# Optimization experiments

Hardware: AMD Instinct MI355X
Metric: run time of the kernel (lower is better)

The kernel has to match this reference:

```python
import jax, jax.numpy as jnp
import numpy as np

DIM = 64
HEADS = 8
GLOBAL_HEADS = 4   # heads - local_attn_heads
DIM_HEAD = 64
INNER = HEADS * DIM_HEAD  # 512
NB_FEATURES = int(DIM_HEAD * np.log(DIM_HEAD))  # 266, performer_pytorch default
NUM_TOKENS = 64
VOCAB = 26
B, N = 8, 2048


def _orth_gauss(m, d, rng):
    # gaussian orthogonal random matrix (scaling=0), as in performer_pytorch
    blocks = []
    for _ in range(int(np.ceil(m / d))):
        q, _ = np.linalg.qr(rng.normal(size=(d, d)))
        blocks.append(q.T)
    mat = np.concatenate(blocks, 0)[:m]
    mult = np.linalg.norm(rng.normal(size=(m, d)), axis=1)
    return (mult[:, None] * mat).astype(np.float32)


def _layernorm(x, g, b, eps=1e-5):
    mu = x.mean(-1, keepdims=True)
    var = jnp.mean((x - mu) ** 2, axis=-1, keepdims=True)
    return (x - mu) / jnp.sqrt(var + eps) * g + b


def _fixed_pos_emb(n, dim):
    inv_freq = 1.0 / (10000.0 ** (jnp.arange(0, dim, 2, dtype=jnp.float32) / dim))
    t = jnp.arange(n, dtype=jnp.float32)[:, None] * inv_freq[None, :]
    return jnp.concatenate([jnp.sin(t), jnp.cos(t)], axis=-1)  # [n, dim]


def _rotate_every_two(x):
    x1, x2 = x[..., ::2], x[..., 1::2]
    return jnp.stack((-x2, x1), axis=-1).reshape(x.shape)


def _apply_rotary(q, k, sinu):
    half = sinu.shape[-1] // 2
    sin = jnp.repeat(sinu[:, :half], 2, axis=-1)
    cos = jnp.repeat(sinu[:, half:], 2, axis=-1)
    rot = lambda t: t * cos + _rotate_every_two(t) * sin
    return rot(q), rot(k)


def _softmax_kernel(x, proj, is_query, eps=1e-4):
    # FAVOR+ positive softmax random features
    dn = x.shape[-1] ** -0.25
    ratio = proj.shape[0] ** -0.5
    dash = jnp.einsum('bhnd,md->bhnm', x * dn, proj)
    diag = jnp.sum(x * x, axis=-1, keepdims=True) * (0.5 * dn * dn)
    mx = jnp.max(dash, axis=-1, keepdims=True) if is_query else jnp.max(dash)
    return ratio * (jnp.exp(dash - diag - mx) + eps)


def _forward(input_ids, tok_emb, ln1_g, ln1_b, Wq, Wk, Wv, Wo, ln2_g, ln2_b,
             W1, b1, W2, b2, lnf_g, lnf_b, Wout, bout, Wc1, bc1, Wc2, bc2, proj):
    b, n = input_ids.shape
    mask = input_ids != 0  # padding mask (pad id == 0)
    x = tok_emb[input_ids] + _fixed_pos_emb(n, DIM)[None]  # token + abs sinusoidal pos
    sinu = _fixed_pos_emb(n, DIM_HEAD)  # rotary table for attention heads

    def attn(h):
        hn = _layernorm(h, ln1_g, ln1_b)
        to_h = lambda W: (hn @ W).reshape(b, n, HEADS, DIM_HEAD).transpose(0, 2, 1, 3)
        q, k, v = to_h(Wq), to_h(Wk), to_h(Wv)  # [b,h,n,d]
        qg, ql = q[:, :GLOBAL_HEADS], q[:, GLOBAL_HEADS:]
        kg, kl = k[:, :GLOBAL_HEADS], k[:, GLOBAL_HEADS:]
        vg, vl = v[:, :GLOBAL_HEADS], v[:, GLOBAL_HEADS:]
        # --- global heads: FAVOR+ linear attention (rotary applied to global q/k only) ---
        vg = vg * mask[:, None, :, None]  # performer zeroes v at padded positions
        qg, kg = _apply_rotary(qg, kg, sinu)
        qp = _softmax_kernel(qg, proj, True)   # [b,h,n,m]
        kp = _softmax_kernel(kg, proj, False)
        ctx = jnp.einsum('bhnm,bhnd->bhmd', kp, vg)
        denom = jnp.einsum('bhnm,bhm->bhn', qp, kp.sum(axis=2))
        og = jnp.einsum('bhnm,bhmd->bhnd', qp, ctx) / denom[..., None]
        # --- local heads: window_size == seq_len -> exact softmax attn + key pad mask ---
        dots = jnp.einsum('bhnd,bhmd->bhnm', ql, kl) * (DIM_HEAD ** -0.5)
        dots = jnp.where(mask[:, None, None, :], dots, jnp.asarray(-1e9, dots.dtype))
        ol = jnp.einsum('bhnm,bhmd->bhnd', jax.nn.softmax(dots, axis=-1), vl)
        out = jnp.concatenate([og, ol], axis=1).transpose(0, 2, 1, 3).reshape(b, n, INNER)
        return out @ Wo

    def ff(h):
        hn = _layernorm(h, ln2_g, ln2_b)
        return jax.nn.gelu(hn @ W1 + b1, approximate=False) @ W2 + b2

    # reversible sequence, depth 1: x1 = x2 = x; output = mean of the two streams
    y1 = x + attn(x)
    y2 = x + ff(y1)
    h = _layernorm(0.5 * (y1 + y2), lnf_g, lnf_b)
    logits = h @ Wout + bout  # [b, n, NUM_TOKENS]
    rep = logits[:, 0, :]     # CLS slot, [b, 64]
    out = jax.nn.relu(rep @ Wc1 + bc1) @ Wc2 + bc2  # [b, 2]
    return out, rep


def setup_inputs():
    key = jax.random.key(0)
    ks = jax.random.split(key, 12)
    rng = np.random.default_rng(0)
    s = lambda k, shape, scale=0.05: jax.random.normal(k, shape, jnp.float32) * scale
    return {
        'input_ids': jax.random.randint(ks[0], (B, N), 0, VOCAB, dtype=jnp.int32),
        'tok_emb': s(ks[1], (NUM_TOKENS, DIM), 1.0),
        'ln1_g': jnp.ones((DIM,), jnp.float32), 'ln1_b': jnp.zeros((DIM,), jnp.float32),
        'Wq': s(ks[2], (DIM, INNER)), 'Wk': s(ks[3], (DIM, INNER)), 'Wv': s(ks[4], (DIM, INNER)),
        'Wo': s(ks[5], (INNER, DIM)),
        'ln2_g': jnp.ones((DIM,), jnp.float32), 'ln2_b': jnp.zeros((DIM,), jnp.float32),
        'W1': s(ks[6], (DIM, 4 * DIM)), 'b1': jnp.zeros((4 * DIM,), jnp.float32),
        'W2': s(ks[7], (4 * DIM, DIM)), 'b2': jnp.zeros((DIM,), jnp.float32),
        'lnf_g': jnp.ones((DIM,), jnp.float32), 'lnf_b': jnp.zeros((DIM,), jnp.float32),
        'Wout': s(ks[8], (DIM, NUM_TOKENS)), 'bout': jnp.zeros((NUM_TOKENS,), jnp.float32),
        'Wc1': s(ks[9], (DIM, 32)), 'bc1': jnp.zeros((32,), jnp.float32),
        'Wc2': s(ks[10], (32, 2)), 'bc2': jnp.zeros((2,), jnp.float32),
        'proj': jnp.asarray(_orth_gauss(NB_FEATURES, DIM_HEAD, rng)),
    }


def reference(input_ids, tok_emb, ln1_g, ln1_b, Wq, Wk, Wv, Wo, ln2_g, ln2_b,
              W1, b1, W2, b2, lnf_g, lnf_b, Wout, bout, Wc1, bc1, Wc2, bc2, proj):
    return _forward(input_ids, tok_emb, ln1_g, ln1_b, Wq, Wk, Wv, Wo, ln2_g, ln2_b,
                    W1, b1, W2, b2, lnf_g, lnf_b, Wout, bout, Wc1, bc1, Wc2, bc2, proj)
```

## Files before the change

### kernel.cpp

```cpp
#include <hip/hip_runtime.h>
#include <math.h>

#define NTOK 2048
#define NBF 266
#define MPAD 272
#define ZWORDS4 138843u

typedef unsigned short u16;
typedef __attribute__((ext_vector_type(8))) short short8;
typedef __attribute__((ext_vector_type(4))) float f32x4;

__device__ __forceinline__ float bf2f(u16 u) {
  unsigned int x = ((unsigned int)u) << 16;
  return __uint_as_float(x);
}
__device__ __forceinline__ u16 f2bf(float f) {
  unsigned int x = __float_as_uint(f);
  unsigned int r = x + 0x7FFFu + ((x >> 16) & 1u);
  return (u16)(r >> 16);
}
__device__ __forceinline__ float wredsum64(float v) {
  for (int o = 32; o > 0; o >>= 1) v += __shfl_xor(v, o);
  return v;
}
__device__ __forceinline__ float bsum256(float v, float* red) {
  for (int o = 32; o > 0; o >>= 1) v += __shfl_xor(v, o);
  __syncthreads();
  if ((threadIdx.x & 63) == 0) red[threadIdx.x >> 6] = v;
  __syncthreads();
  return red[0] + red[1] + red[2] + red[3];
}
__device__ __forceinline__ float bmax256(float v, float* red) {
  for (int o = 32; o > 0; o >>= 1) v = fmaxf(v, __shfl_xor(v, o));
  __syncthreads();
  if ((threadIdx.x & 63) == 0) red[threadIdx.x >> 6] = v;
  __syncthreads();
  return fmaxf(fmaxf(red[0], red[1]), fmaxf(red[2], red[3]));
}
#define INVF_C 0.4152410118609190f

__global__ __launch_bounds__(128) void k_prep(
    const int* __restrict__ ids, const float* __restrict__ tok_emb,
    const float* __restrict__ ln1g, const float* __restrict__ ln1b,
    const float* __restrict__ Wk, const float* __restrict__ Wv,
    u16* __restrict__ Kg, u16* __restrict__ Vg, u16* __restrict__ hng,
    float* __restrict__ diagK, float* __restrict__ x0,
    uint4* __restrict__ zbase) {
  int blk = blockIdx.x;
  int b = blk >> 8, nt = blk & 255;
  int n0 = nt * 8;
  int t = threadIdx.x;
  int w = t >> 6, lane = t & 63;
  __shared__ float hn[8][64];
  __shared__ float idm[8];
  __shared__ float2 sctab[256];

  {
    unsigned int zi = (unsigned int)blk * 128u + (unsigned int)t;
    if (zi < ZWORDS4) zbase[zi] = make_uint4(0u, 0u, 0u, 0u);
  }
#pragma unroll
  for (int p = 0; p < 2; ++p) {
    int ee = t + p * 128;
    int n = n0 + (ee >> 5), i = ee & 31;
    float ang = (float)n * exp2f(-INVF_C * (float)i);
    sctab[ee] = make_float2(sinf(ang), cosf(ang));
  }
  __syncthreads();

  float g = ln1g[lane], bb = ln1b[lane];
#pragma unroll
  for (int j2 = 0; j2 < 4; ++j2) {
    int j = w * 4 + j2;
    int n = n0 + j;
    int id = ids[b * NTOK + n];
    float2 p = sctab[(j << 5) + (lane & 31)];
    float pv = (lane < 32) ? p.x : p.y;
    float xv = tok_emb[id * 64 + lane] + pv;
    float mu = wredsum64(xv) * 0.015625f;
    float dv = xv - mu;
    float var = wredsum64(dv * dv) * 0.015625f;
    float hv = dv * rsqrtf(var + 1e-5f) * g + bb;
    hn[j][lane] = hv;
    hng[((size_t)b * NTOK + n) * 64 + lane] = f2bf(hv);
    if (lane == 0) idm[j] = (id != 0) ? 1.f : 0.f;
    if (n == 0) x0[b * 64 + lane] = xv;
  }
  __syncthreads();

  float acc[8][4];
#pragma unroll
  for (int j = 0; j < 8; ++j)
#pragma unroll
    for (int i = 0; i < 4; ++i) acc[j][i] = 0.f;
  const float* wsrc = (t < 64) ? (Wk + t * 4) : (Wv + (t - 64) * 4);
  for (int d2 = 0; d2 < 64; ++d2) {
    float4 w0 = *reinterpret_cast<const float4*>(wsrc + d2 * 512);
#pragma unroll
    for (int j = 0; j < 8; ++j) {
      float hv = hn[j][d2];
      acc[j][0] += hv * w0.x; acc[j][1] += hv * w0.y;
      acc[j][2] += hv * w0.z; acc[j][3] += hv * w0.w;
    }
  }

  if (t < 64) {
    int hh = t >> 4, db = (t & 15) * 4;
    int i0 = (t & 15) * 2;
#pragma unroll
    for (int j = 0; j < 8; ++j) {
      int n = n0 + j;
      float2 t0 = sctab[(j << 5) + i0];
      float2 t1 = sctab[(j << 5) + i0 + 1];
      float s0 = t0.x, c0 = t0.y, s1 = t1.x, c1 = t1.y;
      float kr0 = acc[j][0] * c0 - acc[j][1] * s0;
      float kr1 = acc[j][1] * c0 + acc[j][0] * s0;
      float kr2 = acc[j][2] * c1 - acc[j][3] * s1;
      float kr3 = acc[j][3] * c1 + acc[j][2] * s1;
      float dq = kr0 * kr0 + kr1 * kr1 + kr2 * kr2 + kr3 * kr3;
      dq += __shfl_xor(dq, 1);
      dq += __shfl_xor(dq, 2);
      dq += __shfl_xor(dq, 4);
      dq += __shfl_xor(dq, 8);
      size_t hb = (size_t)(b * 4 + hh) * NTOK + n;
      if ((t & 15) == 0) diagK[hb] = dq * 0.0625f;
      ushort4 s;
      s.x = f2bf(kr0); s.y = f2bf(kr1); s.z = f2bf(kr2); s.w = f2bf(kr3);
      *reinterpret_cast<ushort4*>(Kg + hb * 64 + db) = s;
    }
  } else {
    int tv = t - 64;
    int hh = tv >> 4, db = (tv & 15) * 4;
#pragma unroll
    for (int j = 0; j < 8; ++j) {
      int n = n0 + j;
      float m = idm[j];
      ushort4 vv;
      vv.x = f2bf(acc[j][0] * m); vv.y = f2bf(acc[j][1] * m);
      vv.z = f2bf(acc[j][2] * m); vv.w = f2bf(acc[j][3] * m);
      *reinterpret_cast<ushort4*>(
          Vg + ((size_t)(b * 4 + hh) * NTOK + n) * 64 + db) = vv;
    }
  }
}

__device__ __forceinline__ void stage_prj(const float* __restrict__ proj,
                                          u16* prjbf, int t, int m0, int rows) {
  for (int c = t; c < rows * 8; c += 256) {
    int r = c >> 3, k0 = (c & 7) * 8;
    int m = m0 + r;
    int e = (r * 64 + k0) ^ ((r & 7) << 3);
    uint4 pk;
    if (m < NBF) {
      const float4* ps = reinterpret_cast<const float4*>(proj + m * 64 + k0);
      float4 p0 = ps[0], p1 = ps[1];
      pk.x = (unsigned)f2bf(p0.x) | ((unsigned)f2bf(p0.y) << 16);
      pk.y = (unsigned)f2bf(p0.z) | ((unsigned)f2bf(p0.w) << 16);
      pk.z = (unsigned)f2bf(p1.x) | ((unsigned)f2bf(p1.y) << 16);
      pk.w = (unsigned)f2bf(p1.z) | ((unsigned)f2bf(p1.w) << 16);
    } else {
      pk.x = pk.y = pk.z = pk.w = 0u;
    }
    *reinterpret_cast<uint4*>(&prjbf[e]) = pk;
  }
}

__global__ __launch_bounds__(256) void k_max(
    const u16* __restrict__ Kg, const float* __restrict__ proj,
    unsigned int* __restrict__ gmax) {
  int bh = blockIdx.x, ns = blockIdx.y;
  int t = threadIdx.x, lane = t & 63, w = t >> 6;
  __shared__ __align__(16) u16 prjbf[MPAD * 64];
  __shared__ __align__(16) u16 kbf[64 * 64];
  __shared__ float red[4];
  stage_prj(proj, prjbf, t, 0, MPAD);
  float mv = -3e38f;
  int ko = (lane >> 4) * 8;
  for (int c4 = 0; c4 < 2; ++c4) {
    int nb = ns * 128 + c4 * 64;
    __syncthreads();
    for (int p = 0; p < 2; ++p) {
      int idx = t + p * 256;
      int n = idx >> 3, k0 = (idx & 7) * 8;
      uint4 src = *reinterpret_cast<const uint4*>(
          Kg + ((size_t)bh * NTOK + nb + n) * 64 + k0);
      *reinterpret_cast<uint4*>(&kbf[(n * 64 + k0) ^ ((n & 7) << 3)]) = src;
    }
    __syncthreads();
    int nl = w * 16 + (lane & 15);
    short8 a0 = *reinterpret_cast<const short8*>(&kbf[(nl * 64 + ko) ^ ((nl & 7) << 3)]);
    short8 a1 = *reinterpret_cast<const short8*>(&kbf[(nl * 64 + ko + 32) ^ ((nl & 7) << 3)]);
#pragma unroll
    for (int mt = 0; mt < 17; ++mt) {
      int m = mt * 16 + (lane & 15);
      short8 b0 = *reinterpret_cast<const short8*>(&prjbf[(m * 64 + ko) ^ ((m & 7) << 3)]);
      short8 b1 = *reinterpret_cast<const short8*>(&prjbf[(m * 64 + ko + 32) ^ ((m & 7) << 3)]);
      f32x4 d = {0.f, 0.f, 0.f, 0.f};
      d = __builtin_amdgcn_mfma_f32_16x16x32_bf16(a0, b0, d, 0, 0, 0);
      d = __builtin_amdgcn_mfma_f32_16x16x32_bf16(a1, b1, d, 0, 0, 0);
      if (m < NBF) {
        mv = fmaxf(mv, fmaxf(fmaxf(d[0], d[1]), fmaxf(d[2], d[3])));
      }
    }
  }
  mv *= 0.35355339059327373f;
  for (int o = 32; o > 0; o >>= 1) mv = fmaxf(mv, __shfl_xor(mv, o));
  __syncthreads();
  if (lane == 0) red[w] = mv;
  __syncthreads();
  if (t == 0) {
    float m2 = fmaxf(fmaxf(red[0], red[1]), fmaxf(red[2], red[3]));
    unsigned int b = __float_as_uint(m2);
    unsigned int u = (b & 0x80000000u) ? ~b : (b | 0x80000000u);
    atomicMax(gmax, u);
  }
}

__global__ __launch_bounds__(256) void k_ctx(
    const u16* __restrict__ Kg, const u16* __restrict__ Vg,
    const float* __restrict__ diagK, const float* __restrict__ proj,
    const unsigned int* __restrict__ gmax,
    float* __restrict__ ctx, float* __restrict__ ksum) {
  int bh = blockIdx.x, ns = blockIdx.y, mz = blockIdx.z;
  int m0 = mz * 144;
  int nmt = mz ? 8 : 9;
  int t = threadIdx.x, lane = t & 63, w = t >> 6;
  __shared__ __align__(16) u16 prjbf[144 * 64];
  __shared__ __align__(16) u16 kpT[144 * 64];
  __shared__ __align__(16) u16 kbf[64 * 64];
  __shared__ __align__(16) u16 vbT[64 * 64];
  __shared__ float dg[64];
  __shared__ float ksl[144];
  stage_prj(proj, prjbf, t, m0, 144);
  if (t < 144) ksl[t] = 0.f;
  unsigned int u = *gmax;
  unsigned int bb = (u & 0x80000000u) ? (u & 0x7FFFFFFFu) : ~u;
  float mx = __uint_as_float(bb);
  const float dn = 0.35355339059327373f;
  const float ratio = 1.0f / sqrtf(266.0f);
  int ko = (lane >> 4) * 8;
  f32x4 acc[9];
  float ksacc[9];
#pragma unroll
  for (int i = 0; i < 9; ++i) { acc[i] = (f32x4){0.f, 0.f, 0.f, 0.f}; ksacc[i] = 0.f; }

  for (int c4 = 0; c4 < 4; ++c4) {
    int nb = ns * 256 + c4 * 64;
    for (int p = 0; p < 2; ++p) {
      int idx = t + p * 256;
      int n = idx >> 3, k0 = (idx & 7) * 8;
      uint4 src = *reinterpret_cast<const uint4*>(
          Kg + ((size_t)bh * NTOK + nb + n) * 64 + k0);
      *reinterpret_cast<uint4*>(&kbf[(n * 64 + k0) ^ ((n & 7) << 3)]) = src;
      uint4 vv = *reinterpret_cast<const uint4*>(
          Vg + ((size_t)bh * NTOK + nb + n) * 64 + k0);
      u16 pv[8];
      *reinterpret_cast<uint4*>(pv) = vv;
#pragma unroll
      for (int i = 0; i < 8; ++i) {
        int d = k0 + i;
        vbT[(d * 64 + n) ^ ((d & 7) << 3)] = pv[i];
      }
    }
    if (t < 64) dg[t] = diagK[(size_t)bh * NTOK + nb + t];
    __syncthreads();
    {
      int nl = w * 16 + (lane & 15);
      short8 a0 = *reinterpret_cast<const short8*>(&kbf[(nl * 64 + ko) ^ ((nl & 7) << 3)]);
      short8 a1 = *reinterpret_cast<const short8*>(&kbf[(nl * 64 + ko + 32) ^ ((nl & 7) << 3)]);
      float dgv[4];
#pragma unroll
      for (int r = 0; r < 4; ++r) dgv[r] = dg[w * 16 + (lane >> 4) * 4 + r];
      int n0 = w * 16 + (lane >> 4) * 4;
#pragma unroll
      for (int mt = 0; mt < 9; ++mt) {
        if (mt < nmt) {
          int lr = mt * 16 + (lane & 15);
          short8 b0 = *reinterpret_cast<const short8*>(&prjbf[(lr * 64 + ko) ^ ((lr & 7) << 3)]);
          short8 b1 = *reinterpret_cast<const short8*>(&prjbf[(lr * 64 + ko + 32) ^ ((lr & 7) << 3)]);
          f32x4 d = {0.f, 0.f, 0.f, 0.f};
          d = __builtin_amdgcn_mfma_f32_16x16x32_bf16(a0, b0, d, 0, 0, 0);
          d = __builtin_amdgcn_mfma_f32_16x16x32_bf16(a1, b1, d, 0, 0, 0);
          float kp0 = ratio * (expf(dn * d[0] - dgv[0] - mx) + 1e-4f);
          float kp1 = ratio * (expf(dn * d[1] - dgv[1] - mx) + 1e-4f);
          float kp2 = ratio * (expf(dn * d[2] - dgv[2] - mx) + 1e-4f);
          float kp3 = ratio * (expf(dn * d[3] - dgv[3] - mx) + 1e-4f);
          ushort4 pkk;
          pkk.x = f2bf(kp0); pkk.y = f2bf(kp1); pkk.z = f2bf(kp2); pkk.w = f2bf(kp3);
          *reinterpret_cast<ushort4*>(&kpT[(lr * 64 + n0) ^ ((lr & 7) << 3)]) = pkk;
          float ksp = kp0 + kp1 + kp2 + kp3;
          ksp += __shfl_xor(ksp, 16);
          ksp += __shfl_xor(ksp, 32);
          ksacc[mt] += ksp;
        }
      }
    }
    __syncthreads();
    {
      int dcol = w * 16 + (lane & 15);
      short8 vb0 = *reinterpret_cast<const short8*>(&vbT[(dcol * 64 + ko) ^ ((dcol & 7) << 3)]);
      short8 vb1 = *reinterpret_cast<const short8*>(&vbT[(dcol * 64 + ko + 32) ^ ((dcol & 7) << 3)]);
#pragma unroll
      for (int mt = 0; mt < 9; ++mt) {
        if (mt < nmt) {
          int lr = mt * 16 + (lane & 15);
          short8 a0 = *reinterpret_cast<const short8*>(&kpT[(lr * 64 + ko) ^ ((lr & 7) << 3)]);
          short8 a1 = *reinterpret_cast<const short8*>(&kpT[(lr * 64 + ko + 32) ^ ((lr & 7) << 3)]);
          acc[mt] = __builtin_amdgcn_mfma_f32_16x16x32_bf16(a0, vb0, acc[mt], 0, 0, 0);
          acc[mt] = __builtin_amdgcn_mfma_f32_16x16x32_bf16(a1, vb1, acc[mt], 0, 0, 0);
        }
      }
    }
    __syncthreads();
  }
  int dcol = w * 16 + (lane & 15);
#pragma unroll
  for (int mt = 0; mt < 9; ++mt) {
    if (mt < nmt) {
#pragma unroll
      for (int r = 0; r < 4; ++r) {
        int m = m0 + mt * 16 + (lane >> 4) * 4 + r;
        if (m < NBF)
          atomicAdd(&ctx[((size_t)bh * NBF + m) * 64 + dcol], acc[mt][r]);
      }
      if (lane < 16) atomicAdd(&ksl[mt * 16 + lane], ksacc[mt]);
    }
  }
  __syncthreads();
  if (t < 144 && m0 + t < NBF)
    atomicAdd(&ksum[(size_t)bh * NBF + m0 + t], ksl[t]);
}

__global__ __launch_bounds__(256) void k_att(
    const int* __restrict__ ids,
    const float* __restrict__ ln1g, const float* __restrict__ ln1b,
    const float* __restrict__ Wq, const float* __restrict__ Wk,
    const float* __restrict__ Wv, const float* __restrict__ proj,
    const u16* __restrict__ hng,
    const float* __restrict__ ctx, const float* __restrict__ ksum,
    const float* __restrict__ x0,
    const float* __restrict__ ln2g, const float* __restrict__ ln2b,
    const float* __restrict__ Wo,
    const float* __restrict__ W1, const float* __restrict__ b1,
    const float* __restrict__ W2, const float* __restrict__ b2,
    const float* __restrict__ lnfg, const float* __restrict__ lnfb,
    const float* __restrict__ Wout, const float* __restrict__ bout,
    const float* __restrict__ Wc1, const float* __restrict__ bc1,
    const float* __restrict__ Wc2, const float* __restrict__ bc2,
    float* __restrict__ att, float* __restrict__ svecG,
    float* __restrict__ sdenG, unsigned int* __restrict__ cnt,
    float* __restrict__ out) {
  int b = blockIdx.x, y = blockIdx.y;
  int t = threadIdx.x, lane = t & 63, wg = t >> 6;
  __shared__ float hn1[64], qh[64], qpart[4][64], red[4], pol[4][64];
  __shared__ float buf[272];
  __shared__ __align__(16) u16 vst[512 * 64];
  __shared__ float pbuf[512];
  __shared__ float wkq[64];
  __shared__ int lastf;
  __shared__ float fo512[512], fx0[64], fy1[64], fhn2[64], fgact[256];
  __shared__ float fhfin[64], frep[64], fc1[32], fsd[4];
  const float dn = 0.35355339059327373f;
  const float ratio = 1.0f / sqrtf(266.0f);
  int h = (y < 4) ? y : (4 + ((y - 4) >> 2));

  if (t < 64) {
    float xv = x0[b * 64 + t];
    float mu = wredsum64(xv) * 0.015625f;
    float dv = xv - mu;
    float var = wredsum64(dv * dv) * 0.015625f;
    hn1[t] = dv * rsqrtf(var + 1e-5f) * ln1g[t] + ln1b[t];
  }
  __syncthreads();
  {
    float p = 0;
#pragma unroll
    for (int dd = 0; dd < 16; ++dd)
      p += hn1[wg * 16 + dd] * Wq[(wg * 16 + dd) * 512 + h * 64 + lane];
    qpart[wg][lane] = p;
  }
  __syncthreads();
  if (t < 64) qh[t] = qpart[0][t] + qpart[1][t] + qpart[2][t] + qpart[3][t];
  __syncthreads();

  if (y < 4) {
    int bh = b * 4 + h;
    float dq = 0;
#pragma unroll
    for (int d = 0; d < 64; ++d) dq += qh[d] * qh[d];
    dq *= 0.0625f;
    float lmax = -3e38f;
#pragma unroll
    for (int pass = 0; pass < 2; ++pass) {
      int m = t + pass * 256;
      if (m < NBF) {
        const float4* pp = reinterpret_cast<const float4*>(proj + m * 64);
        float s = 0;
#pragma unroll
        for (int q4 = 0; q4 < 16; ++q4) {
          float4 uu = pp[q4];
          s += qh[q4 * 4] * uu.x + qh[q4 * 4 + 1] * uu.y +
               qh[q4 * 4 + 2] * uu.z + qh[q4 * 4 + 3] * uu.w;
        }
        float dash = dn * s;
        buf[m] = dash;
        lmax = fmaxf(lmax, dash);
      }
    }
    float mxq = bmax256(lmax, red);
    float part = 0;
#pragma unroll
    for (int pass = 0; pass < 2; ++pass) {
      int m = t + pass * 256;
      if (m < NBF) {
        float qp = ratio * (expf(buf[m] - dq - mxq) + 1e-4f);
        buf[m] = qp;
        part += qp * ksum[(size_t)bh * NBF + m];
      }
    }
    float den = bsum256(part, red);
    __syncthreads();
    {
      float s = 0;
      for (int m = wg; m < NBF; m += 4)
        s += buf[m] * ctx[((size_t)bh * NBF + m) * 64 + lane];
      pol[wg][lane] = s;
    }
    __syncthreads();
    if (t < 64)
      att[b * 512 + h * 64 + t] =
          (pol[0][t] + pol[1][t] + pol[2][t] + pol[3][t]) / den;
  } else {
    int hl = (y - 4) >> 2, sl = (y - 4) & 3;
    int ch = (4 + hl) * 64;
    {
      float p = 0;
#pragma unroll
      for (int jj = 0; jj < 16; ++jj)
        p += Wk[lane * 512 + ch + wg * 16 + jj] * qh[wg * 16 + jj];
      qpart[wg][lane] = p;
    }
    __syncthreads();
    if (t < 64) wkq[t] = qpart[0][t] + qpart[1][t] + qpart[2][t] + qpart[3][t];
    const u16* hnb = hng + ((size_t)b * NTOK + sl * 512) * 64;
    for (int p = 0; p < 16; ++p) {
      int idx = t + p * 256;
      int r = idx >> 3, k0 = (idx & 7) * 8;
      uint4 src = *reinterpret_cast<const uint4*>(hnb + (size_t)r * 64 + k0);
      *reinterpret_cast<uint4*>(&vst[(r * 64 + k0) ^ ((r & 7) << 3)]) = src;
    }
    __syncthreads();
    float ps = 0;
#pragma unroll
    for (int i = 0; i < 2; ++i) {
      int r = t + i * 256;
      float s = 0;
#pragma unroll
      for (int c8 = 0; c8 < 8; ++c8) {
        uint4 uu = *reinterpret_cast<const uint4*>(
            &vst[(r * 64 + c8 * 8) ^ ((r & 7) << 3)]);
        u16 pv[8];
        *reinterpret_cast<uint4*>(pv) = uu;
#pragma unroll
        for (int k = 0; k < 8; ++k) s += wkq[c8 * 8 + k] * bf2f(pv[k]);
      }
      float p = (ids[b * NTOK + sl * 512 + r] == 0) ? 0.f : expf(s * 0.125f);
      pbuf[r] = p;
      ps += p;
    }
    float psb = bsum256(ps, red);
    if (t == 0) atomicAdd(&sdenG[b * 4 + hl], psb);
    float acc = 0;
    int r0 = wg * 128;
#pragma unroll 8
    for (int r = 0; r < 128; ++r)
      acc += pbuf[r0 + r] * bf2f(vst[((r0 + r) * 64 + lane) ^ (((r0 + r) & 7) << 3)]);
    pol[wg][lane] = acc;
    __syncthreads();
    if (t < 64)
      atomicAdd(&svecG[(b * 4 + hl) * 64 + t],
                pol[0][t] + pol[1][t] + pol[2][t] + pol[3][t]);
  }

  __syncthreads();
  if (t == 0) {
    __threadfence();
    unsigned int prev = atomicAdd(&cnt[b], 1u);
    lastf = (prev == 19u) ? 1 : 0;
  }
  __syncthreads();
  if (!lastf) return;
  __threadfence();

  if (t < 4) fsd[t] = sdenG[b * 4 + t];
  {
    int hh = t >> 6, j = t & 63;
    float s = 0;
#pragma unroll 8
    for (int d = 0; d < 64; ++d)
      s += svecG[(b * 4 + hh) * 64 + d] * Wv[d * 512 + 256 + hh * 64 + j];
    pol[hh][j] = s;
  }
  if (t < 256) fo512[t] = att[b * 512 + t];
  if (t < 64) fx0[t] = x0[b * 64 + t];
  __syncthreads();
  {
    int hh = t >> 6, j = t & 63;
    fo512[256 + hh * 64 + j] = pol[hh][j] / fsd[hh];
  }
  __syncthreads();
  {
    float s = 0;
#pragma unroll 4
    for (int c = wg * 128; c < wg * 128 + 128; ++c) s += fo512[c] * Wo[c * 64 + lane];
    pol[wg][lane] = s;
  }
  __syncthreads();
  if (t < 64) {
    float yv = fx0[t] + pol[0][t] + pol[1][t] + pol[2][t] + pol[3][t];
    fy1[t] = yv;
    float mu = wredsum64(yv) * 0.015625f;
    float dv = yv - mu;
    float var = wredsum64(dv * dv) * 0.015625f;
    fhn2[t] = dv * rsqrtf(var + 1e-5f) * ln2g[t] + ln2b[t];
  }
  __syncthreads();
  {
    float s = b1[t];
#pragma unroll 4
    for (int d = 0; d < 64; ++d) s += fhn2[d] * W1[d * 256 + t];
    fgact[t] = 0.5f * s * (1.f + erff(s * 0.7071067811865475f));
  }
  __syncthreads();
  {
    float s = 0;
#pragma unroll 4
    for (int j = wg * 64; j < wg * 64 + 64; ++j) s += fgact[j] * W2[j * 64 + lane];
    pol[wg][lane] = s;
  }
  __syncthreads();
  if (t < 64) {
    float y2 = fx0[t] + b2[t] + pol[0][t] + pol[1][t] + pol[2][t] + pol[3][t];
    float hm = 0.5f * (fy1[t] + y2);
    float mu = wredsum64(hm) * 0.015625f;
    float dv = hm - mu;
    float var = wredsum64(dv * dv) * 0.015625f;
    fhfin[t] = dv * rsqrtf(var + 1e-5f) * lnfg[t] + lnfb[t];
  }
  __syncthreads();
  {
    float s = 0;
#pragma unroll
    for (int dd = 0; dd < 16; ++dd)
      s += fhfin[wg * 16 + dd] * Wout[(wg * 16 + dd) * 64 + lane];
    pol[wg][lane] = s;
  }
  __syncthreads();
  if (t < 64) {
    float s = bout[t] + pol[0][t] + pol[1][t] + pol[2][t] + pol[3][t];
    frep[t] = s;
    out[16 + b * 64 + t] = s;
  }
  __syncthreads();
  if (t < 32) {
    float s = bc1[t];
#pragma unroll 4
    for (int d = 0; d < 64; ++d) s += frep[d] * Wc1[d * 32 + t];
    fc1[t] = fmaxf(s, 0.f);
  }
  __syncthreads();
  if (t < 2) {
    float s = bc2[t];
#pragma unroll
    for (int jj = 0; jj < 32; ++jj) s += fc1[jj] * Wc2[jj * 2 + t];
    out[b * 2 + t] = s;
  }
}

extern "C" void kernel_launch(void* const* d_in, const int* in_sizes, int n_in,
                              void* d_out, int out_size, void* d_ws, size_t ws_size,
                              hipStream_t stream) {
  (void)in_sizes; (void)n_in; (void)out_size; (void)ws_size;
  const int* ids = (const int*)d_in[0];
  const float* tok = (const float*)d_in[1];
  const float* ln1g = (const float*)d_in[2];
  const float* ln1b = (const float*)d_in[3];
  const float* Wq = (const float*)d_in[4];
  const float* Wk = (const float*)d_in[5];
  const float* Wv = (const float*)d_in[6];
  const float* Wo = (const float*)d_in[7];
  const float* ln2g = (const float*)d_in[8];
  const float* ln2b = (const float*)d_in[9];
  const float* W1 = (const float*)d_in[10];
  const float* b1 = (const float*)d_in[11];
  const float* W2 = (const float*)d_in[12];
  const float* b2 = (const float*)d_in[13];
  const float* lnfg = (const float*)d_in[14];
  const float* lnfb = (const float*)d_in[15];
  const float* Wout = (const float*)d_in[16];
  const float* bout = (const float*)d_in[17];
  const float* Wc1 = (const float*)d_in[18];
  const float* bc1 = (const float*)d_in[19];
  const float* Wc2 = (const float*)d_in[20];
  const float* bc2 = (const float*)d_in[21];
  const float* proj = (const float*)d_in[22];

  uint8_t* w = (uint8_t*)d_ws;
  size_t off = 0;
  const size_t big = (size_t)8 * 4 * NTOK * 64 * 2;
  u16* Kg = (u16*)(w + off); off += big;
  u16* Vg = (u16*)(w + off); off += big;
  u16* hng = (u16*)(w + off); off += (size_t)8 * NTOK * 64 * 2;
  float* diagK = (float*)(w + off); off += (size_t)8 * 4 * NTOK * 4;
  float* ctx = (float*)(w + off); off += (size_t)8 * 4 * NBF * 64 * 4;
  float* ksum = (float*)(w + off); off += (size_t)8 * 4 * NBF * 4;
  float* svecG = (float*)(w + off); off += (size_t)8 * 4 * 64 * 4;
  float* sdenG = (float*)(w + off); off += (size_t)8 * 4 * 4;
  unsigned int* gmax = (unsigned int*)(w + off); off += 4;
  unsigned int* cnt = (unsigned int*)(w + off); off += 32;
  off += 12;
  float* x0 = (float*)(w + off); off += 64 * 8 * 4;
  float* att = (float*)(w + off); off += (size_t)8 * 512 * 4;

  k_prep<<<8 * 256, 128, 0, stream>>>(ids, tok, ln1g, ln1b, Wk, Wv, Kg, Vg, hng,
                                      diagK, x0, (uint4*)ctx);
  k_max<<<dim3(32, 16), 256, 0, stream>>>(Kg, proj, gmax);
  k_ctx<<<dim3(32, 8, 2), 256, 0, stream>>>(Kg, Vg, diagK, proj, gmax, ctx, ksum);
  k_att<<<dim3(8, 20), 256, 0, stream>>>(ids, ln1g, ln1b, Wq, Wk, Wv, proj, hng,
                                         ctx, ksum, x0, ln2g, ln2b, Wo, W1, b1,
                                         W2, b2, lnfg, lnfb, Wout, bout, Wc1,
                                         bc1, Wc2, bc2, att, svecG, sdenG, cnt,
                                         (float*)d_out);
}
```

Baseline: 114.8 us.

## Move local-attention blocks into the context kernel to overlap with FAVOR work

The local-head attention blocks, which compute the query projection, scores over a 512-token slice and the weighted value sum, move out of the final attention kernel into extra z-slices of the context kernel. They now run alongside the FAVOR+ context accumulation, and the final kernel launches only 4 global-head blocks per batch, with the last-block counter adjusted to match. The context kernel's shared memory is merged into a single 64KB buffer reused by both paths. This shortens the serialized tail kernel, at the cost of a larger context-kernel grid with many early-exit blocks and higher shared memory per block, which may lower occupancy.

```diff
diff --git a/kernel.cpp b/kernel.cpp
--- a/kernel.cpp
+++ b/kernel.cpp
@@ -220,17 +220,100 @@
     const u16* __restrict__ Kg, const u16* __restrict__ Vg,
     const float* __restrict__ diagK, const float* __restrict__ proj,
     const unsigned int* __restrict__ gmax,
-    float* __restrict__ ctx, float* __restrict__ ksum) {
+    float* __restrict__ ctx, float* __restrict__ ksum,
+    const int* __restrict__ ids,
+    const float* __restrict__ ln1g, const float* __restrict__ ln1b,
+    const float* __restrict__ Wq, const float* __restrict__ Wk,
+    const float* __restrict__ x0, const u16* __restrict__ hng,
+    float* __restrict__ svecG, float* __restrict__ sdenG) {
   int bh = blockIdx.x, ns = blockIdx.y, mz = blockIdx.z;
+  int t = threadIdx.x, lane = t & 63, w = t >> 6;
+  __shared__ __align__(16) unsigned char bigbuf[65536];
+  __shared__ float dg[64];
+  __shared__ float ksl[144];
+  __shared__ float hn1[64], qh[64], wkq[64], qpart[4][64], red[4], pol[4][64];
+  __shared__ float pbuf[512];
+
+  if (mz == 2) {
+    if (ns >= 4) return;
+    int b = bh >> 2, hl = bh & 3, sl = ns;
+    int ch = (4 + hl) * 64;
+    u16* vst = (u16*)bigbuf;
+    if (t < 64) {
+      float xv = x0[b * 64 + t];
+      float mu = wredsum64(xv) * 0.015625f;
+      float dv = xv - mu;
+      float var = wredsum64(dv * dv) * 0.015625f;
+      hn1[t] = dv * rsqrtf(var + 1e-5f) * ln1g[t] + ln1b[t];
+    }
+    __syncthreads();
+    {
+      float p = 0;
+#pragma unroll
+      for (int dd = 0; dd < 16; ++dd)
+        p += hn1[w * 16 + dd] * Wq[(w * 16 + dd) * 512 + ch + lane];
+      qpart[w][lane] = p;
+    }
+    __syncthreads();
+    if (t < 64) qh[t] = qpart[0][t] + qpart[1][t] + qpart[2][t] + qpart[3][t];
+    __syncthreads();
+    {
+      float p = 0;
+#pragma unroll
+      for (int jj = 0; jj < 16; ++jj)
+        p += Wk[lane * 512 + ch + w * 16 + jj] * qh[w * 16 + jj];
+      qpart[w][lane] = p;
+    }
+    __syncthreads();
+    if (t < 64) wkq[t] = qpart[0][t] + qpart[1][t] + qpart[2][t] + qpart[3][t];
+    const u16* hnb = hng + ((size_t)b * NTOK + sl * 512) * 64;
+#pragma unroll
+    for (int p = 0; p < 16; ++p) {
+      int idx = t + p * 256;
+      int r = idx >> 3, k0 = (idx & 7) * 8;
+      uint4 src = *reinterpret_cast<const uint4*>(hnb + (size_t)r * 64 + k0);
+      *reinterpret_cast<uint4*>(&vst[(r * 64 + k0) ^ ((r & 7) << 3)]) = src;
+    }
+    __syncthreads();
+    float ps = 0;
+#pragma unroll
+    for (int i = 0; i < 2; ++i) {
+      int r = t + i * 256;
+      float s = 0;
+#pragma unroll
+      for (int c8 = 0; c8 < 8; ++c8) {
+        uint4 uu = *reinterpret_cast<const uint4*>(
+            &vst[(r * 64 + c8 * 8) ^ ((r & 7) << 3)]);
+        u16 pv[8];
+        *reinterpret_cast<uint4*>(pv) = uu;
+#pragma unroll
+        for (int k = 0; k < 8; ++k) s += wkq[c8 * 8 + k] * bf2f(pv[k]);
+      }
+      float p = (ids[b * NTOK + sl * 512 + r] == 0) ? 0.f : expf(s * 0.125f);
+      pbuf[r] = p;
+      ps += p;
+    }
+    float psb = bsum256(ps, red);
+    if (t == 0) atomicAdd(&sdenG[b * 4 + hl], psb);
+    float acc = 0;
+    int r0 = w * 128;
+#pragma unroll 8
+    for (int r = 0; r < 128; ++r)
+      acc += pbuf[r0 + r] * bf2f(vst[((r0 + r) * 64 + lane) ^ (((r0 + r) & 7) << 3)]);
+    pol[w][lane] = acc;
+    __syncthreads();
+    if (t < 64)
+      atomicAdd(&svecG[(b * 4 + hl) * 64 + t],
+                pol[0][t] + pol[1][t] + pol[2][t] + pol[3][t]);
+    return;
+  }
+
+  u16* prjbf = (u16*)bigbuf;
+  u16* kpT = (u16*)(bigbuf + 18432);
+  u16* kbf = (u16*)(bigbuf + 36864);
+  u16* vbT = (u16*)(bigbuf + 45056);
   int m0 = mz * 144;
   int nmt = mz ? 8 : 9;
-  int t = threadIdx.x, lane = t & 63, w = t >> 6;
-  __shared__ __align__(16) u16 prjbf[144 * 64];
-  __shared__ __align__(16) u16 kpT[144 * 64];
-  __shared__ __align__(16) u16 kbf[64 * 64];
-  __shared__ __align__(16) u16 vbT[64 * 64];
-  __shared__ float dg[64];
-  __shared__ float ksl[144];
   stage_prj(proj, prjbf, t, m0, 144);
   if (t < 144) ksl[t] = 0.f;
   unsigned int u = *gmax;
@@ -331,12 +414,10 @@
     atomicAdd(&ksum[(size_t)bh * NBF + m0 + t], ksl[t]);
 }
 
-__global__ __launch_bounds__(256) void k_att(
-    const int* __restrict__ ids,
+__global__ __launch_bounds__(256) void k_gatt(
     const float* __restrict__ ln1g, const float* __restrict__ ln1b,
-    const float* __restrict__ Wq, const float* __restrict__ Wk,
-    const float* __restrict__ Wv, const float* __restrict__ proj,
-    const u16* __restrict__ hng,
+    const float* __restrict__ Wq, const float* __restrict__ Wv,
+    const float* __restrict__ proj,
     const float* __restrict__ ctx, const float* __restrict__ ksum,
     const float* __restrict__ x0,
     const float* __restrict__ ln2g, const float* __restrict__ ln2b,
@@ -347,22 +428,18 @@
     const float* __restrict__ Wout, const float* __restrict__ bout,
     const float* __restrict__ Wc1, const float* __restrict__ bc1,
     const float* __restrict__ Wc2, const float* __restrict__ bc2,
-    float* __restrict__ att, float* __restrict__ svecG,
-    float* __restrict__ sdenG, unsigned int* __restrict__ cnt,
+    float* __restrict__ att, const float* __restrict__ svecG,
+    const float* __restrict__ sdenG, unsigned int* __restrict__ cnt,
     float* __restrict__ out) {
-  int b = blockIdx.x, y = blockIdx.y;
+  int b = blockIdx.x, h = blockIdx.y;
   int t = threadIdx.x, lane = t & 63, wg = t >> 6;
   __shared__ float hn1[64], qh[64], qpart[4][64], red[4], pol[4][64];
   __shared__ float buf[272];
-  __shared__ __align__(16) u16 vst[512 * 64];
-  __shared__ float pbuf[512];
-  __shared__ float wkq[64];
   __shared__ int lastf;
   __shared__ float fo512[512], fx0[64], fy1[64], fhn2[64], fgact[256];
   __shared__ float fhfin[64], frep[64], fc1[32], fsd[4];
   const float dn = 0.35355339059327373f;
   const float ratio = 1.0f / sqrtf(266.0f);
-  int h = (y < 4) ? y : (4 + ((y - 4) >> 2));
 
   if (t < 64) {
     float xv = x0[b * 64 + t];
@@ -383,7 +460,7 @@
   if (t < 64) qh[t] = qpart[0][t] + qpart[1][t] + qpart[2][t] + qpart[3][t];
   __syncthreads();
 
-  if (y < 4) {
+  {
     int bh = b * 4 + h;
     float dq = 0;
 #pragma unroll
@@ -430,63 +507,13 @@
     if (t < 64)
       att[b * 512 + h * 64 + t] =
           (pol[0][t] + pol[1][t] + pol[2][t] + pol[3][t]) / den;
-  } else {
-    int hl = (y - 4) >> 2, sl = (y - 4) & 3;
-    int ch = (4 + hl) * 64;
-    {
-      float p = 0;
-#pragma unroll
-      for (int jj = 0; jj < 16; ++jj)
-        p += Wk[lane * 512 + ch + wg * 16 + jj] * qh[wg * 16 + jj];
-      qpart[wg][lane] = p;
-    }
-    __syncthreads();
-    if (t < 64) wkq[t] = qpart[0][t] + qpart[1][t] + qpart[2][t] + qpart[3][t];
-    const u16* hnb = hng + ((size_t)b * NTOK + sl * 512) * 64;
-    for (int p = 0; p < 16; ++p) {
-      int idx = t + p * 256;
-      int r = idx >> 3, k0 = (idx & 7) * 8;
-      uint4 src = *reinterpret_cast<const uint4*>(hnb + (size_t)r * 64 + k0);
-      *reinterpret_cast<uint4*>(&vst[(r * 64 + k0) ^ ((r & 7) << 3)]) = src;
-    }
-    __syncthreads();
-    float ps = 0;
-#pragma unroll
-    for (int i = 0; i < 2; ++i) {
-      int r = t + i * 256;
-      float s = 0;
-#pragma unroll
-      for (int c8 = 0; c8 < 8; ++c8) {
-        uint4 uu = *reinterpret_cast<const uint4*>(
-            &vst[(r * 64 + c8 * 8) ^ ((r & 7) << 3)]);
-        u16 pv[8];
-        *reinterpret_cast<uint4*>(pv) = uu;
-#pragma unroll
-        for (int k = 0; k < 8; ++k) s += wkq[c8 * 8 + k] * bf2f(pv[k]);
-      }
-      float p = (ids[b * NTOK + sl * 512 + r] == 0) ? 0.f : expf(s * 0.125f);
-      pbuf[r] = p;
-      ps += p;
-    }
-    float psb = bsum256(ps, red);
-    if (t == 0) atomicAdd(&sdenG[b * 4 + hl], psb);
-    float acc = 0;
-    int r0 = wg * 128;
-#pragma unroll 8
-    for (int r = 0; r < 128; ++r)
-      acc += pbuf[r0 + r] * bf2f(vst[((r0 + r) * 64 + lane) ^ (((r0 + r) & 7) << 3)]);
-    pol[wg][lane] = acc;
-    __syncthreads();
-    if (t < 64)
-      atomicAdd(&svecG[(b * 4 + hl) * 64 + t],
-                pol[0][t] + pol[1][t] + pol[2][t] + pol[3][t]);
   }
 
   __syncthreads();
   if (t == 0) {
     __threadfence();
     unsigned int prev = atomicAdd(&cnt[b], 1u);
-    lastf = (prev == 19u) ? 1 : 0;
+    lastf = (prev == 3u) ? 1 : 0;
   }
   __syncthreads();
   if (!lastf) return;
@@ -625,10 +652,11 @@
   k_prep<<<8 * 256, 128, 0, stream>>>(ids, tok, ln1g, ln1b, Wk, Wv, Kg, Vg, hng,
                                       diagK, x0, (uint4*)ctx);
   k_max<<<dim3(32, 16), 256, 0, stream>>>(Kg, proj, gmax);
-  k_ctx<<<dim3(32, 8, 2), 256, 0, stream>>>(Kg, Vg, diagK, proj, gmax, ctx, ksum);
-  k_att<<<dim3(8, 20), 256, 0, stream>>>(ids, ln1g, ln1b, Wq, Wk, Wv, proj, hng,
-                                         ctx, ksum, x0, ln2g, ln2b, Wo, W1, b1,
-                                         W2, b2, lnfg, lnfb, Wout, bout, Wc1,
-                                         bc1, Wc2, bc2, att, svecG, sdenG, cnt,
-                                         (float*)d_out);
-}
+  k_ctx<<<dim3(32, 8, 3), 256, 0, stream>>>(Kg, Vg, diagK, proj, gmax, ctx, ksum,
+                                            ids, ln1g, ln1b, Wq, Wk, x0, hng,
+                                            svecG, sdenG);
+  k_gatt<<<dim3(8, 4), 256, 0, stream>>>(ln1g, ln1b, Wq, Wv, proj, ctx, ksum, x0,
+                                         ln2g, ln2b, Wo, W1, b1, W2, b2, lnfg,
+                                         lnfb, Wout, bout, Wc1, bc1, Wc2, bc2,
+                                         att, svecG, sdenG, cnt, (float*)d_out);
+}
```

New measurement: 127.8 us. 11.3% more time.
